# Kernel optimization log

Measured on AMD Instinct MI355X. Metric: run time of the kernel, lower is better.

Reference implementation:

```python
import jax, jax.numpy as jnp
import numpy as np

LOG_PROB_FACTOR = 0.5  # logProbFactor


def setup_inputs() -> dict:
    key = jax.random.key(0)
    ks = jax.random.split(key, 8)
    B, L, F, K = 2048, 512, 64, 2
    s = jax.random.randint(ks[0], (B, L), 0, K)
    W0 = jax.random.normal(ks[1], (K, F), jnp.float32) / np.sqrt(K).astype(np.float32)
    b0 = jnp.zeros((F,), jnp.float32)
    # fused LSTM weights, gate order (i, f, g, o); flax: dense_i no bias, dense_h has bias
    Wi = jax.random.normal(ks[2], (F, 4 * F), jnp.float32) / np.sqrt(F).astype(np.float32)
    Wh = jax.random.normal(ks[3], (F, 4 * F), jnp.float32) / np.sqrt(F).astype(np.float32)
    bh = jnp.zeros((4 * F,), jnp.float32)
    Wa = jax.random.normal(ks[4], (F, K), jnp.float32) / np.sqrt(F).astype(np.float32)
    ba = jnp.zeros((K,), jnp.float32)
    Wp = jax.random.normal(ks[5], (F, 1), jnp.float32) / np.sqrt(F).astype(np.float32)
    bp = jnp.zeros((1,), jnp.float32)
    return {"s": s, "W0": W0, "b0": b0, "Wi": Wi, "Wh": Wh, "bh": bh,
            "Wa": Wa, "ba": ba, "Wp": Wp, "bp": bp}


def _forward(s, W0, b0, Wi, Wh, bh, Wa, ba, Wp, bp):
    B, L = s.shape
    K, F = W0.shape
    # pad a leading zero token: input at step t is spin at site t-1
    s_pad = jnp.pad(s, ((0, 0), (1, 0)))                       # [B, L+1]
    x = jax.nn.one_hot(s_pad, K, dtype=W0.dtype) @ W0 + b0     # layer0: [B, L+1, F]
    xs = jnp.swapaxes(x, 0, 1)                                 # [L+1, B, F] time-major
    c0 = jnp.zeros((B, F), x.dtype)
    h0 = jnp.zeros((B, F), x.dtype)

    def step(carry, xt):
        c, h = carry
        g = xt @ Wi + h @ Wh + bh                              # [B, 4F]
        i, f, gg, o = jnp.split(g, 4, axis=-1)
        cn = jax.nn.sigmoid(f) * c + jax.nn.sigmoid(i) * jnp.tanh(gg)
        hn = jax.nn.sigmoid(o) * jnp.tanh(cn)
        return (cn, hn), hn

    _, ys = jax.lax.scan(step, (c0, h0), xs)                   # [L+1, B, F]

    logits = ys[:-1] @ Wa + ba                                 # [L, B, K]
    logp = jax.nn.log_softmax(logits, axis=-1) * LOG_PROB_FACTOR
    picked = jnp.take_along_axis(logp, s.T[..., None], axis=-1)[..., 0]  # [L, B]
    amp = picked.sum(axis=0)                                   # [B]
    phase = (ys[-1] @ Wp + bp)[..., 0]                         # [B]
    return amp + 1j * phase                                    # complex log-psi per sample


def reference(s, W0, b0, Wi, Wh, bh, Wa, ba, Wp, bp):
    return _forward(s, W0, b0, Wi, Wh, bh, Wa, ba, Wp, bp)
```

## Files before the change

kernel.cpp:

```cpp
#include <hip/hip_runtime.h>
#include <math.h>

typedef _Float16 f16x8 __attribute__((ext_vector_type(8)));
typedef float    f32x4 __attribute__((ext_vector_type(4)));
typedef _Float16 f16x2 __attribute__((ext_vector_type(2)));
typedef __fp16   fp16x2 __attribute__((ext_vector_type(2)));

#define B_TOT 2048
#define LSEQ  512
#define NS    16
#define LOG2E 1.44269504088896f
#define LN2   0.69314718055995f

#define MFMA16(A, B, C) __builtin_amdgcn_mfma_f32_16x16x32_f16((A), (B), (C), 0, 0, 0)

__device__ __forceinline__ unsigned int pkrtz(float a, float b) {
    fp16x2 p = __builtin_amdgcn_cvt_pkrtz(a, b);
    return __builtin_bit_cast(unsigned int, p);
}

__global__ __launch_bounds__(256, 1)
void lstm_v13_kernel(const int* __restrict__ s,
                     const float* __restrict__ W0, const float* __restrict__ b0,
                     const float* __restrict__ Wi, const float* __restrict__ Wh,
                     const float* __restrict__ bh, const float* __restrict__ Wa,
                     const float* __restrict__ ba, const float* __restrict__ Wp,
                     const float* __restrict__ bp, float* __restrict__ out)
{
    const int tid  = threadIdx.x;
    const int w    = tid >> 6;
    const int lane = tid & 63;
    const int n    = lane & 15;
    const int q    = lane >> 4;
    const int b0s  = blockIdx.x * NS;

    __shared__ __align__(16) unsigned int HhD[2][512];
    __shared__ unsigned short TOKB[LSEQ + 2];
    __shared__ unsigned char  SRAW[NS][LSEQ];
    __shared__ _Float16 DBUF[LSEQ][NS];
    __shared__ float PART[16][NS];

    for (int i = tid; i < NS * LSEQ; i += 256)
        SRAW[i >> 9][i & 511] = (unsigned char)s[(b0s + (i >> 9)) * LSEQ + (i & 511)];
    __syncthreads();
    for (int u = tid; u <= LSEQ; u += 256) {
        unsigned int mask = 0;
        if (u >= 1) {
            #pragma unroll
            for (int m = 0; m < NS; ++m)
                mask |= ((unsigned int)SRAW[m][u - 1]) << m;
        }
        TOKB[u] = (unsigned short)mask;
    }

    f16x8 awh[4][2];
    #pragma unroll
    for (int g = 0; g < 4; ++g) {
        const float sc  = (g == 2) ? (2.0f * LOG2E) : (-LOG2E);
        const int   col = 64 * g + 16 * w + n;
        #pragma unroll
        for (int c = 0; c < 2; ++c)
            #pragma unroll
            for (int j = 0; j < 8; ++j)
                awh[g][c][j] = (_Float16)(Wh[(32 * c + 8 * q + j) * 256 + col] * sc);
    }

    f16x8 awd[2];
    #pragma unroll
    for (int c = 0; c < 2; ++c)
        #pragma unroll
        for (int j = 0; j < 8; ++j) {
            int k = 32 * c + 8 * q + j;
            awd[c][j] = (_Float16)((n == 0) ? (Wa[2 * k + 1] - Wa[2 * k]) : 0.0f);
        }
    const float dba = ba[1] - ba[0];

    f32x4 p0q[4], dpq[4];
    {
        float a0[4][4], a1[4][4];
        #pragma unroll
        for (int g = 0; g < 4; ++g)
            #pragma unroll
            for (int r = 0; r < 4; ++r) {
                float bb = bh[64 * g + 16 * w + 4 * q + r];
                a0[g][r] = bb; a1[g][r] = bb;
            }
        for (int f = 0; f < 64; ++f) {
            float wb0 = W0[f]      + b0[f];
            float wb1 = W0[64 + f] + b0[f];
            #pragma unroll
            for (int g = 0; g < 4; ++g) {
                const float4 wi4 = *(const float4*)&Wi[f * 256 + 64 * g + 16 * w + 4 * q];
                #pragma unroll
                for (int r = 0; r < 4; ++r) {
                    float wi = (&wi4.x)[r];
                    a0[g][r] = fmaf(wb0, wi, a0[g][r]);
                    a1[g][r] = fmaf(wb1, wi, a1[g][r]);
                }
            }
        }
        #pragma unroll
        for (int g = 0; g < 4; ++g) {
            const float sc = (g == 2) ? (2.0f * LOG2E) : (-LOG2E);
            #pragma unroll
            for (int r = 0; r < 4; ++r) {
                p0q[g][r] = a0[g][r] * sc;
                dpq[g][r] = (a1[g][r] - a0[g][r]) * sc;
            }
        }
    }

    __syncthreads();

    const int wAddr = 4 * n + 64 * (q >> 1) + 128 * w + 2 * (q & 1);
    const int rAddr = 4 * n + 64 * (q & 1) + 128 * (q >> 1);

    float h4[4] = {0, 0, 0, 0}, c4[4] = {0, 0, 0, 0};
    f32x4 ci[4];
    #pragma unroll
    for (int g = 0; g < 4; ++g) ci[g] = p0q[g];

    float dpend = 0.0f;
    int   tpend = -1;

    #pragma unroll 4
    for (int v = 0; v <= LSEQ; ++v) {
        const int p = v & 1;
        unsigned int* __restrict__ hb = &HhD[p][0];

        uint2 hw;
        hw.x = pkrtz(h4[0], h4[1]);
        hw.y = pkrtz(h4[2], h4[3]);
        *(uint2*)&hb[wAddr] = hw;
        __syncthreads();

        if (tpend >= 0) {
            if (lane < 16) DBUF[tpend][n] = (_Float16)dpend;
            tpend = -1;
        }

        uint4 r0 = *(const uint4*)&hb[rAddr];
        uint4 r1 = *(const uint4*)&hb[rAddr + 256];
        const f16x8 bf0 = __builtin_bit_cast(f16x8, r0);
        const f16x8 bf1 = __builtin_bit_cast(f16x8, r1);

        const unsigned int tokm_next = (v < LSEQ) ? (unsigned int)TOKB[v + 1] : 0u;

        f32x4 acc0 = ci[0], acc1 = ci[1], acc2 = ci[2], acc3 = ci[3];
        acc0 = MFMA16(awh[0][0], bf0, acc0);
        acc1 = MFMA16(awh[1][0], bf0, acc1);
        acc2 = MFMA16(awh[2][0], bf0, acc2);
        acc3 = MFMA16(awh[3][0], bf0, acc3);
        acc0 = MFMA16(awh[0][1], bf1, acc0);
        acc1 = MFMA16(awh[1][1], bf1, acc1);
        acc2 = MFMA16(awh[2][1], bf1, acc2);
        acc3 = MFMA16(awh[3][1], bf1, acc3);

        if (v >= 1 && w == (v & 3)) {
            f32x4 da = (f32x4){dba, dba, dba, dba};
            da = MFMA16(awd[0], bf0, da);
            da = MFMA16(awd[1], bf1, da);
            dpend = da[0];
            tpend = v - 1;
        }

        const float sel = (float)((tokm_next >> n) & 1u);
        const f32x4 sel4 = {sel, sel, sel, sel};
        #pragma unroll
        for (int g = 0; g < 4; ++g)
            ci[g] = dpq[g] * sel4 + p0q[g];

        #pragma unroll
        for (int r = 0; r < 4; ++r) {
            float ei = __builtin_amdgcn_exp2f(acc0[r]);
            float ef = __builtin_amdgcn_exp2f(acc1[r]);
            float eg = __builtin_amdgcn_exp2f(acc2[r]);
            float eo = __builtin_amdgcn_exp2f(acc3[r]);
            float P  = (1.0f + ei) * (eg + 1.0f);
            float F  = 1.0f + ef;
            float R2 = __builtin_amdgcn_rcpf(P * F);
            float cn = fmaf(c4[r] * P, R2, (eg - 1.0f) * F * R2);
            c4[r] = cn;
            float ec = __builtin_amdgcn_exp2f(fminf(cn * (2.0f * LOG2E), 60.f));
            float Ro = __builtin_amdgcn_rcpf((1.0f + eo) * (ec + 1.0f));
            h4[r] = (ec - 1.0f) * Ro;
        }
    }

    if (tpend >= 0 && lane < 16) DBUF[tpend][n] = (_Float16)dpend;
    {
        uint2 hw;
        hw.x = pkrtz(h4[0], h4[1]);
        hw.y = pkrtz(h4[2], h4[3]);
        *(uint2*)&HhD[1][wAddr] = hw;
    }
    __syncthreads();

    {
        const int nn = tid & 15;
        const int ch = tid >> 4;
        float a = 0.0f;
        #pragma unroll 4
        for (int k = 0; k < 32; ++k) {
            int t = ch * 32 + k;
            float d = (float)DBUF[t][nn];
            float x = SRAW[nn][t] ? -d : d;
            float e = __builtin_amdgcn_exp2f(-fabsf(x) * LOG2E);
            a += fmaxf(x, 0.0f) + __builtin_amdgcn_logf(1.0f + e) * LN2;
        }
        PART[ch][nn] = a;
    }
    __syncthreads();

    if (tid < 16) {
        float ssum = 0.0f;
        #pragma unroll
        for (int c = 0; c < 16; ++c) ssum += PART[c][tid];
        out[b0s + tid] = -0.5f * ssum;
    }

    if (w == 0) {
        float ph = 0.0f;
        #pragma unroll
        for (int d = 0; d < 4; ++d) {
            unsigned int ua = HhD[1][4 * n + 128 * q + d];
            unsigned int ub = HhD[1][4 * n + 64 + 128 * q + d];
            f16x2 ha  = __builtin_bit_cast(f16x2, ua);
            f16x2 hb2 = __builtin_bit_cast(f16x2, ub);
            ph = fmaf((float)ha[0], Wp[16 * q + 2 * d],
                 fmaf((float)ha[1], Wp[16 * q + 2 * d + 1], ph));
            ph = fmaf((float)hb2[0], Wp[16 * q + 8 + 2 * d],
                 fmaf((float)hb2[1], Wp[16 * q + 8 + 2 * d + 1], ph));
        }
        ph += __shfl_xor(ph, 16, 64);
        ph += __shfl_xor(ph, 32, 64);
        if (q == 0) out[B_TOT + b0s + n] = ph + bp[0];
    }
}

extern "C" void kernel_launch(void* const* d_in, const int* in_sizes, int n_in,
                              void* d_out, int out_size, void* d_ws, size_t ws_size,
                              hipStream_t stream) {
    const int*   s  = (const int*)  d_in[0];
    const float* W0 = (const float*)d_in[1];
    const float* b0 = (const float*)d_in[2];
    const float* Wi = (const float*)d_in[3];
    const float* Wh = (const float*)d_in[4];
    const float* bh = (const float*)d_in[5];
    const float* Wa = (const float*)d_in[6];
    const float* ba = (const float*)d_in[7];
    const float* Wp = (const float*)d_in[8];
    const float* bp = (const float*)d_in[9];
    float* out = (float*)d_out;

    dim3 grid(B_TOT / NS);
    dim3 block(256);
    lstm_v13_kernel<<<grid, block, 0, stream>>>(s, W0, b0, Wi, Wh, bh,
                                                Wa, ba, Wp, bp, out);
}
```

Measured before the change: 320.7 us.

## Pack two independent 16-sample LSTM chains into each 512-thread block

Each block now runs two independent groups of 16 batch samples, one per 256-thread half, with separate shared-memory buffers indexed by chain. This halves the grid and doubles the block size, so each CU interleaves two recurrence chains and can hide the latency of MFMA, transcendental and LDS operations in the serial time loop. In exchange, the block-wide barrier now couples both chains every step, and fewer CUs are used overall.

```diff
diff --git a/kernel.cpp b/kernel.cpp
--- a/kernel.cpp
+++ b/kernel.cpp
@@ -9,6 +9,7 @@
 #define B_TOT 2048
 #define LSEQ  512
 #define NS    16
+#define NCH   2
 #define LOG2E 1.44269504088896f
 #define LN2   0.69314718055995f
 
@@ -19,8 +20,8 @@
     return __builtin_bit_cast(unsigned int, p);
 }
 
-__global__ __launch_bounds__(256, 1)
-void lstm_v13_kernel(const int* __restrict__ s,
+__global__ __launch_bounds__(512, 1)
+void lstm_v14_kernel(const int* __restrict__ s,
                      const float* __restrict__ W0, const float* __restrict__ b0,
                      const float* __restrict__ Wi, const float* __restrict__ Wh,
                      const float* __restrict__ bh, const float* __restrict__ Wa,
@@ -28,29 +29,31 @@
                      const float* __restrict__ bp, float* __restrict__ out)
 {
     const int tid  = threadIdx.x;
-    const int w    = tid >> 6;
+    const int ch   = tid >> 8;
+    const int ct   = tid & 255;
+    const int w    = ct >> 6;
     const int lane = tid & 63;
     const int n    = lane & 15;
     const int q    = lane >> 4;
-    const int b0s  = blockIdx.x * NS;
-
-    __shared__ __align__(16) unsigned int HhD[2][512];
-    __shared__ unsigned short TOKB[LSEQ + 2];
-    __shared__ unsigned char  SRAW[NS][LSEQ];
-    __shared__ _Float16 DBUF[LSEQ][NS];
-    __shared__ float PART[16][NS];
-
-    for (int i = tid; i < NS * LSEQ; i += 256)
-        SRAW[i >> 9][i & 511] = (unsigned char)s[(b0s + (i >> 9)) * LSEQ + (i & 511)];
-    __syncthreads();
-    for (int u = tid; u <= LSEQ; u += 256) {
+    const int b0s  = blockIdx.x * (NS * NCH) + ch * NS;
+
+    __shared__ __align__(16) unsigned int HhD[NCH][2][512];
+    __shared__ unsigned short TOKB[NCH][LSEQ + 2];
+    __shared__ unsigned char  SRAW[NCH][NS][LSEQ];
+    __shared__ _Float16 DBUF[NCH][LSEQ][NS];
+    __shared__ float PART[NCH][16][NS];
+
+    for (int i = ct; i < NS * LSEQ; i += 256)
+        SRAW[ch][i >> 9][i & 511] = (unsigned char)s[(b0s + (i >> 9)) * LSEQ + (i & 511)];
+    __syncthreads();
+    for (int u = ct; u <= LSEQ; u += 256) {
         unsigned int mask = 0;
         if (u >= 1) {
             #pragma unroll
             for (int m = 0; m < NS; ++m)
-                mask |= ((unsigned int)SRAW[m][u - 1]) << m;
-        }
-        TOKB[u] = (unsigned short)mask;
+                mask |= ((unsigned int)SRAW[ch][m][u - 1]) << m;
+        }
+        TOKB[ch][u] = (unsigned short)mask;
     }
 
     f16x8 awh[4][2];
@@ -126,7 +129,7 @@
     #pragma unroll 4
     for (int v = 0; v <= LSEQ; ++v) {
         const int p = v & 1;
-        unsigned int* __restrict__ hb = &HhD[p][0];
+        unsigned int* __restrict__ hb = &HhD[ch][p][0];
 
         uint2 hw;
         hw.x = pkrtz(h4[0], h4[1]);
@@ -135,7 +138,7 @@
         __syncthreads();
 
         if (tpend >= 0) {
-            if (lane < 16) DBUF[tpend][n] = (_Float16)dpend;
+            if (lane < 16) DBUF[ch][tpend][n] = (_Float16)dpend;
             tpend = -1;
         }
 
@@ -144,7 +147,7 @@
         const f16x8 bf0 = __builtin_bit_cast(f16x8, r0);
         const f16x8 bf1 = __builtin_bit_cast(f16x8, r1);
 
-        const unsigned int tokm_next = (v < LSEQ) ? (unsigned int)TOKB[v + 1] : 0u;
+        const unsigned int tokm_next = (v < LSEQ) ? (unsigned int)TOKB[ch][v + 1] : 0u;
 
         f32x4 acc0 = ci[0], acc1 = ci[1], acc2 = ci[2], acc3 = ci[3];
         acc0 = MFMA16(awh[0][0], bf0, acc0);
@@ -187,44 +190,44 @@
         }
     }
 
-    if (tpend >= 0 && lane < 16) DBUF[tpend][n] = (_Float16)dpend;
+    if (tpend >= 0 && lane < 16) DBUF[ch][tpend][n] = (_Float16)dpend;
     {
         uint2 hw;
         hw.x = pkrtz(h4[0], h4[1]);
         hw.y = pkrtz(h4[2], h4[3]);
-        *(uint2*)&HhD[1][wAddr] = hw;
+        *(uint2*)&HhD[ch][1][wAddr] = hw;
     }
     __syncthreads();
 
     {
-        const int nn = tid & 15;
-        const int ch = tid >> 4;
+        const int nn = ct & 15;
+        const int cc = ct >> 4;
         float a = 0.0f;
         #pragma unroll 4
         for (int k = 0; k < 32; ++k) {
-            int t = ch * 32 + k;
-            float d = (float)DBUF[t][nn];
-            float x = SRAW[nn][t] ? -d : d;
+            int t = cc * 32 + k;
+            float d = (float)DBUF[ch][t][nn];
+            float x = SRAW[ch][nn][t] ? -d : d;
             float e = __builtin_amdgcn_exp2f(-fabsf(x) * LOG2E);
             a += fmaxf(x, 0.0f) + __builtin_amdgcn_logf(1.0f + e) * LN2;
         }
-        PART[ch][nn] = a;
-    }
-    __syncthreads();
-
-    if (tid < 16) {
+        PART[ch][cc][nn] = a;
+    }
+    __syncthreads();
+
+    if (ct < 16) {
         float ssum = 0.0f;
         #pragma unroll
-        for (int c = 0; c < 16; ++c) ssum += PART[c][tid];
-        out[b0s + tid] = -0.5f * ssum;
+        for (int c = 0; c < 16; ++c) ssum += PART[ch][c][ct];
+        out[b0s + ct] = -0.5f * ssum;
     }
 
     if (w == 0) {
         float ph = 0.0f;
         #pragma unroll
         for (int d = 0; d < 4; ++d) {
-            unsigned int ua = HhD[1][4 * n + 128 * q + d];
-            unsigned int ub = HhD[1][4 * n + 64 + 128 * q + d];
+            unsigned int ua = HhD[ch][1][4 * n + 128 * q + d];
+            unsigned int ub = HhD[ch][1][4 * n + 64 + 128 * q + d];
             f16x2 ha  = __builtin_bit_cast(f16x2, ua);
             f16x2 hb2 = __builtin_bit_cast(f16x2, ub);
             ph = fmaf((float)ha[0], Wp[16 * q + 2 * d],
@@ -253,8 +256,8 @@
     const float* bp = (const float*)d_in[9];
     float* out = (float*)d_out;
 
-    dim3 grid(B_TOT / NS);
-    dim3 block(256);
-    lstm_v13_kernel<<<grid, block, 0, stream>>>(s, W0, b0, Wi, Wh, bh,
+    dim3 grid(B_TOT / (NS * NCH));
+    dim3 block(512);
+    lstm_v14_kernel<<<grid, block, 0, stream>>>(s, W0, b0, Wi, Wh, bh,
                                                 Wa, ba, Wp, bp, out);
 }
```

Result: slower. 425.5 us (+32.7%).

## Halve samples per block to double grid and split gate math across lanes

Applied to the files above, without the earlier changes.

Each block now handles 8 samples instead of 16, which doubles the grid to 256 blocks so every CU on the device gets work. The 16-column MFMA tile is reused with duplicated sample columns. Each lane now computes the nonlinear gate math for only 2 of its 4 accumulator rows, selected by the high bit of the column index, which halves the per-step elementwise work. The cost is that half of the MFMA throughput is spent on duplicate columns, and the reduction and DBUF indexing change with it.

```diff
diff --git a/kernel.cpp b/kernel.cpp
--- a/kernel.cpp
+++ b/kernel.cpp
@@ -8,7 +8,7 @@
 
 #define B_TOT 2048
 #define LSEQ  512
-#define NS    16
+#define NS    8
 #define LOG2E 1.44269504088896f
 #define LN2   0.69314718055995f
 
@@ -20,7 +20,7 @@
 }
 
 __global__ __launch_bounds__(256, 1)
-void lstm_v13_kernel(const int* __restrict__ s,
+void lstm_v16_kernel(const int* __restrict__ s,
                      const float* __restrict__ W0, const float* __restrict__ b0,
                      const float* __restrict__ Wi, const float* __restrict__ Wh,
                      const float* __restrict__ bh, const float* __restrict__ Wa,
@@ -32,13 +32,15 @@
     const int lane = tid & 63;
     const int n    = lane & 15;
     const int q    = lane >> 4;
+    const int ns   = n & 7;
+    const int hi   = n >> 3;
     const int b0s  = blockIdx.x * NS;
 
     __shared__ __align__(16) unsigned int HhD[2][512];
     __shared__ unsigned short TOKB[LSEQ + 2];
     __shared__ unsigned char  SRAW[NS][LSEQ];
     __shared__ _Float16 DBUF[LSEQ][NS];
-    __shared__ float PART[16][NS];
+    __shared__ float PART[32][NS];
 
     for (int i = tid; i < NS * LSEQ; i += 256)
         SRAW[i >> 9][i & 511] = (unsigned char)s[(b0s + (i >> 9)) * LSEQ + (i & 511)];
@@ -112,10 +114,10 @@
 
     __syncthreads();
 
-    const int wAddr = 4 * n + 64 * (q >> 1) + 128 * w + 2 * (q & 1);
-    const int rAddr = 4 * n + 64 * (q & 1) + 128 * (q >> 1);
-
-    float h4[4] = {0, 0, 0, 0}, c4[4] = {0, 0, 0, 0};
+    const int wAddr = 4 * ns + 64 * (q >> 1) + 128 * w + 2 * (q & 1) + hi;
+    const int rAddr = 4 * ns + 64 * (q & 1) + 128 * (q >> 1);
+
+    float h2[2] = {0, 0}, c2[2] = {0, 0};
     f32x4 ci[4];
     #pragma unroll
     for (int g = 0; g < 4; ++g) ci[g] = p0q[g];
@@ -128,14 +130,11 @@
         const int p = v & 1;
         unsigned int* __restrict__ hb = &HhD[p][0];
 
-        uint2 hw;
-        hw.x = pkrtz(h4[0], h4[1]);
-        hw.y = pkrtz(h4[2], h4[3]);
-        *(uint2*)&hb[wAddr] = hw;
+        hb[wAddr] = pkrtz(h2[0], h2[1]);
         __syncthreads();
 
         if (tpend >= 0) {
-            if (lane < 16) DBUF[tpend][n] = (_Float16)dpend;
+            if (lane < 8) DBUF[tpend][lane] = (_Float16)dpend;
             tpend = -1;
         }
 
@@ -164,58 +163,59 @@
             tpend = v - 1;
         }
 
-        const float sel = (float)((tokm_next >> n) & 1u);
+        const float sel = (float)((tokm_next >> ns) & 1u);
         const f32x4 sel4 = {sel, sel, sel, sel};
         #pragma unroll
         for (int g = 0; g < 4; ++g)
             ci[g] = dpq[g] * sel4 + p0q[g];
 
-        #pragma unroll
-        for (int r = 0; r < 4; ++r) {
-            float ei = __builtin_amdgcn_exp2f(acc0[r]);
-            float ef = __builtin_amdgcn_exp2f(acc1[r]);
-            float eg = __builtin_amdgcn_exp2f(acc2[r]);
-            float eo = __builtin_amdgcn_exp2f(acc3[r]);
+        const bool hb2 = (hi != 0);
+        float gi[2] = { hb2 ? acc0[2] : acc0[0], hb2 ? acc0[3] : acc0[1] };
+        float gf[2] = { hb2 ? acc1[2] : acc1[0], hb2 ? acc1[3] : acc1[1] };
+        float gg[2] = { hb2 ? acc2[2] : acc2[0], hb2 ? acc2[3] : acc2[1] };
+        float go[2] = { hb2 ? acc3[2] : acc3[0], hb2 ? acc3[3] : acc3[1] };
+
+        #pragma unroll
+        for (int rr = 0; rr < 2; ++rr) {
+            float ei = __builtin_amdgcn_exp2f(gi[rr]);
+            float ef = __builtin_amdgcn_exp2f(gf[rr]);
+            float eg = __builtin_amdgcn_exp2f(gg[rr]);
+            float eo = __builtin_amdgcn_exp2f(go[rr]);
             float P  = (1.0f + ei) * (eg + 1.0f);
             float F  = 1.0f + ef;
             float R2 = __builtin_amdgcn_rcpf(P * F);
-            float cn = fmaf(c4[r] * P, R2, (eg - 1.0f) * F * R2);
-            c4[r] = cn;
+            float cn = fmaf(c2[rr] * P, R2, (eg - 1.0f) * F * R2);
+            c2[rr] = cn;
             float ec = __builtin_amdgcn_exp2f(fminf(cn * (2.0f * LOG2E), 60.f));
             float Ro = __builtin_amdgcn_rcpf((1.0f + eo) * (ec + 1.0f));
-            h4[r] = (ec - 1.0f) * Ro;
-        }
-    }
-
-    if (tpend >= 0 && lane < 16) DBUF[tpend][n] = (_Float16)dpend;
+            h2[rr] = (ec - 1.0f) * Ro;
+        }
+    }
+
+    if (tpend >= 0 && lane < 8) DBUF[tpend][lane] = (_Float16)dpend;
+    HhD[1][wAddr] = pkrtz(h2[0], h2[1]);
+    __syncthreads();
+
     {
-        uint2 hw;
-        hw.x = pkrtz(h4[0], h4[1]);
-        hw.y = pkrtz(h4[2], h4[3]);
-        *(uint2*)&HhD[1][wAddr] = hw;
-    }
-    __syncthreads();
-
-    {
-        const int nn = tid & 15;
-        const int ch = tid >> 4;
+        const int nn = tid & 7;
+        const int cp = tid >> 3;
         float a = 0.0f;
         #pragma unroll 4
-        for (int k = 0; k < 32; ++k) {
-            int t = ch * 32 + k;
+        for (int k = 0; k < 16; ++k) {
+            int t = cp * 16 + k;
             float d = (float)DBUF[t][nn];
             float x = SRAW[nn][t] ? -d : d;
             float e = __builtin_amdgcn_exp2f(-fabsf(x) * LOG2E);
             a += fmaxf(x, 0.0f) + __builtin_amdgcn_logf(1.0f + e) * LN2;
         }
-        PART[ch][nn] = a;
-    }
-    __syncthreads();
-
-    if (tid < 16) {
+        PART[cp][nn] = a;
+    }
+    __syncthreads();
+
+    if (tid < 8) {
         float ssum = 0.0f;
         #pragma unroll
-        for (int c = 0; c < 16; ++c) ssum += PART[c][tid];
+        for (int c = 0; c < 32; ++c) ssum += PART[c][tid];
         out[b0s + tid] = -0.5f * ssum;
     }
 
@@ -223,18 +223,18 @@
         float ph = 0.0f;
         #pragma unroll
         for (int d = 0; d < 4; ++d) {
-            unsigned int ua = HhD[1][4 * n + 128 * q + d];
-            unsigned int ub = HhD[1][4 * n + 64 + 128 * q + d];
+            unsigned int ua = HhD[1][4 * ns + 128 * q + d];
+            unsigned int ub = HhD[1][4 * ns + 64 + 128 * q + d];
             f16x2 ha  = __builtin_bit_cast(f16x2, ua);
-            f16x2 hb2 = __builtin_bit_cast(f16x2, ub);
+            f16x2 hc  = __builtin_bit_cast(f16x2, ub);
             ph = fmaf((float)ha[0], Wp[16 * q + 2 * d],
                  fmaf((float)ha[1], Wp[16 * q + 2 * d + 1], ph));
-            ph = fmaf((float)hb2[0], Wp[16 * q + 8 + 2 * d],
-                 fmaf((float)hb2[1], Wp[16 * q + 8 + 2 * d + 1], ph));
+            ph = fmaf((float)hc[0], Wp[16 * q + 8 + 2 * d],
+                 fmaf((float)hc[1], Wp[16 * q + 8 + 2 * d + 1], ph));
         }
         ph += __shfl_xor(ph, 16, 64);
         ph += __shfl_xor(ph, 32, 64);
-        if (q == 0) out[B_TOT + b0s + n] = ph + bp[0];
+        if (q == 0 && n < 8) out[B_TOT + b0s + n] = ph + bp[0];
     }
 }
 
@@ -255,6 +255,6 @@
 
     dim3 grid(B_TOT / NS);
     dim3 block(256);
-    lstm_v13_kernel<<<grid, block, 0, stream>>>(s, W0, b0, Wi, Wh, bh,
+    lstm_v16_kernel<<<grid, block, 0, stream>>>(s, W0, b0, Wi, Wh, bh,
                                                 Wa, ba, Wp, bp, out);
 }
```

Result: faster. 277.1 us (-13.6%).

## Give each wavefront two independent sequences to drop per-step block barriers

Applied to the files above, without the earlier changes.

Before, four wavefronts split the gate columns for 16 sequences and had to sync at a block barrier on every timestep. Now each wavefront owns two sequences outright and holds all 16 gate tiles of Wh in registers. The hidden state is exchanged only through wave-private LDS, so the per-step __syncthreads disappears. The cost is 32 MFMAs per step for just two sequences, which wastes most of the MFMA N dimension, plus much higher register pressure. The grid grows to 256 blocks of 8 sequences.

```diff
diff --git a/kernel.cpp b/kernel.cpp
--- a/kernel.cpp
+++ b/kernel.cpp
@@ -3,12 +3,10 @@
 
 typedef _Float16 f16x8 __attribute__((ext_vector_type(8)));
 typedef float    f32x4 __attribute__((ext_vector_type(4)));
-typedef _Float16 f16x2 __attribute__((ext_vector_type(2)));
 typedef __fp16   fp16x2 __attribute__((ext_vector_type(2)));
 
 #define B_TOT 2048
 #define LSEQ  512
-#define NS    16
 #define LOG2E 1.44269504088896f
 #define LN2   0.69314718055995f
 
@@ -18,9 +16,15 @@
     fp16x2 p = __builtin_amdgcn_cvt_pkrtz(a, b);
     return __builtin_bit_cast(unsigned int, p);
 }
+__device__ __forceinline__ float f16lo(unsigned int u) {
+    return (float)__builtin_bit_cast(fp16x2, u)[0];
+}
+__device__ __forceinline__ float f16hi(unsigned int u) {
+    return (float)__builtin_bit_cast(fp16x2, u)[1];
+}
 
 __global__ __launch_bounds__(256, 1)
-void lstm_v13_kernel(const int* __restrict__ s,
+void lstm_v17_kernel(const int* __restrict__ s,
                      const float* __restrict__ W0, const float* __restrict__ b0,
                      const float* __restrict__ Wi, const float* __restrict__ Wh,
                      const float* __restrict__ bh, const float* __restrict__ Wa,
@@ -32,209 +36,186 @@
     const int lane = tid & 63;
     const int n    = lane & 15;
     const int q    = lane >> 4;
-    const int b0s  = blockIdx.x * NS;
-
-    __shared__ __align__(16) unsigned int HhD[2][512];
-    __shared__ unsigned short TOKB[LSEQ + 2];
-    __shared__ unsigned char  SRAW[NS][LSEQ];
-    __shared__ _Float16 DBUF[LSEQ][NS];
-    __shared__ float PART[16][NS];
-
-    for (int i = tid; i < NS * LSEQ; i += 256)
-        SRAW[i >> 9][i & 511] = (unsigned char)s[(b0s + (i >> 9)) * LSEQ + (i & 511)];
-    __syncthreads();
-    for (int u = tid; u <= LSEQ; u += 256) {
-        unsigned int mask = 0;
-        if (u >= 1) {
-            #pragma unroll
-            for (int m = 0; m < NS; ++m)
-                mask |= ((unsigned int)SRAW[m][u - 1]) << m;
-        }
-        TOKB[u] = (unsigned short)mask;
-    }
-
-    f16x8 awh[4][2];
+    const int ns   = n & 1;
+    const int kcpy = n >> 1;
+    const int c    = kcpy >> 1;
+    const int p    = kcpy & 1;
+    const int b0s  = blockIdx.x * 8 + w * 2;
+
+    __shared__ __align__(16) unsigned int HWX[4 * 64];
+    __shared__ unsigned char TOKW[4][LSEQ + 4];
+    __shared__ _Float16 DBUF[4][LSEQ][2];
+
     #pragma unroll
-    for (int g = 0; g < 4; ++g) {
-        const float sc  = (g == 2) ? (2.0f * LOG2E) : (-LOG2E);
-        const int   col = 64 * g + 16 * w + n;
-        #pragma unroll
-        for (int c = 0; c < 2; ++c)
-            #pragma unroll
-            for (int j = 0; j < 8; ++j)
-                awh[g][c][j] = (_Float16)(Wh[(32 * c + 8 * q + j) * 256 + col] * sc);
-    }
-
-    f16x8 awd[2];
-    #pragma unroll
-    for (int c = 0; c < 2; ++c)
-        #pragma unroll
-        for (int j = 0; j < 8; ++j) {
-            int k = 32 * c + 8 * q + j;
-            awd[c][j] = (_Float16)((n == 0) ? (Wa[2 * k + 1] - Wa[2 * k]) : 0.0f);
-        }
-    const float dba = ba[1] - ba[0];
-
-    f32x4 p0q[4], dpq[4];
+    for (int j = 0; j < 8; ++j) {
+        int t = lane + 64 * j;
+        int s0 = s[(b0s + 0) * LSEQ + t];
+        int s1 = s[(b0s + 1) * LSEQ + t];
+        TOKW[w][t] = (unsigned char)(s0 | (s1 << 1));
+    }
+    if (lane == 0) TOKW[w][LSEQ] = 0;
+
+    f32x4 p0q[16], dpq[16];
     {
-        float a0[4][4], a1[4][4];
-        #pragma unroll
-        for (int g = 0; g < 4; ++g)
+        f32x4 A0[16], A1[16];
+        #pragma unroll
+        for (int t = 0; t < 16; ++t)
             #pragma unroll
             for (int r = 0; r < 4; ++r) {
-                float bb = bh[64 * g + 16 * w + 4 * q + r];
-                a0[g][r] = bb; a1[g][r] = bb;
+                float bb = bh[16 * t + 4 * q + r];
+                A0[t][r] = bb; A1[t][r] = bb;
             }
+        #pragma unroll 2
         for (int f = 0; f < 64; ++f) {
             float wb0 = W0[f]      + b0[f];
             float wb1 = W0[64 + f] + b0[f];
             #pragma unroll
-            for (int g = 0; g < 4; ++g) {
-                const float4 wi4 = *(const float4*)&Wi[f * 256 + 64 * g + 16 * w + 4 * q];
+            for (int t = 0; t < 16; ++t) {
+                const float4 wi4 = *(const float4*)&Wi[f * 256 + 16 * t + 4 * q];
                 #pragma unroll
                 for (int r = 0; r < 4; ++r) {
-                    float wi = (&wi4.x)[r];
-                    a0[g][r] = fmaf(wb0, wi, a0[g][r]);
-                    a1[g][r] = fmaf(wb1, wi, a1[g][r]);
+                    float wv = (&wi4.x)[r];
+                    A0[t][r] = fmaf(wb0, wv, A0[t][r]);
+                    A1[t][r] = fmaf(wb1, wv, A1[t][r]);
                 }
             }
         }
         #pragma unroll
-        for (int g = 0; g < 4; ++g) {
-            const float sc = (g == 2) ? (2.0f * LOG2E) : (-LOG2E);
+        for (int t = 0; t < 16; ++t) {
+            const float sc = ((t >> 2) == 2) ? (2.0f * LOG2E) : (-LOG2E);
             #pragma unroll
             for (int r = 0; r < 4; ++r) {
-                p0q[g][r] = a0[g][r] * sc;
-                dpq[g][r] = (a1[g][r] - a0[g][r]) * sc;
+                p0q[t][r] = A0[t][r] * sc;
+                dpq[t][r] = (A1[t][r] - A0[t][r]) * sc;
             }
         }
     }
 
-    __syncthreads();
-
-    const int wAddr = 4 * n + 64 * (q >> 1) + 128 * w + 2 * (q & 1);
-    const int rAddr = 4 * n + 64 * (q & 1) + 128 * (q >> 1);
-
-    float h4[4] = {0, 0, 0, 0}, c4[4] = {0, 0, 0, 0};
-    f32x4 ci[4];
+    f16x8 awh[16][2];
     #pragma unroll
-    for (int g = 0; g < 4; ++g) ci[g] = p0q[g];
-
-    float dpend = 0.0f;
-    int   tpend = -1;
-
-    #pragma unroll 4
+    for (int t = 0; t < 16; ++t) {
+        const float sc = ((t >> 2) == 2) ? (2.0f * LOG2E) : (-LOG2E);
+        const int col = 16 * t + n;
+        #pragma unroll
+        for (int h = 0; h < 2; ++h)
+            #pragma unroll
+            for (int j = 0; j < 8; ++j)
+                awh[t][h][j] = (_Float16)(Wh[(32 * h + 8 * q + j) * 256 + col] * sc);
+    }
+    f16x8 awd[2];
+    #pragma unroll
+    for (int h = 0; h < 2; ++h)
+        #pragma unroll
+        for (int j = 0; j < 8; ++j) {
+            int kx = 32 * h + 8 * q + j;
+            awd[h][j] = (_Float16)((n == 0) ? (Wa[2 * kx + 1] - Wa[2 * kx]) : 0.0f);
+        }
+    const float dba = ba[1] - ba[0];
+
+    const int wA  = w * 64 + 32 * ns + 8 * c + 2 * q + p;
+    const int rA0 = w * 64 + 32 * ns + 4 * q;
+
+    float h2[2] = {0.f, 0.f}, c2[2] = {0.f, 0.f};
+    float selc = 0.f;
+
     for (int v = 0; v <= LSEQ; ++v) {
-        const int p = v & 1;
-        unsigned int* __restrict__ hb = &HhD[p][0];
-
-        uint2 hw;
-        hw.x = pkrtz(h4[0], h4[1]);
-        hw.y = pkrtz(h4[2], h4[3]);
-        *(uint2*)&hb[wAddr] = hw;
-        __syncthreads();
-
-        if (tpend >= 0) {
-            if (lane < 16) DBUF[tpend][n] = (_Float16)dpend;
-            tpend = -1;
-        }
-
-        uint4 r0 = *(const uint4*)&hb[rAddr];
-        uint4 r1 = *(const uint4*)&hb[rAddr + 256];
+        HWX[wA] = pkrtz(h2[0], h2[1]);
+        const unsigned int tk = TOKW[w][v];
+        const uint4 r0 = *(const uint4*)&HWX[rA0];
+        const uint4 r1 = *(const uint4*)&HWX[rA0 + 16];
         const f16x8 bf0 = __builtin_bit_cast(f16x8, r0);
         const f16x8 bf1 = __builtin_bit_cast(f16x8, r1);
 
-        const unsigned int tokm_next = (v < LSEQ) ? (unsigned int)TOKB[v + 1] : 0u;
-
-        f32x4 acc0 = ci[0], acc1 = ci[1], acc2 = ci[2], acc3 = ci[3];
-        acc0 = MFMA16(awh[0][0], bf0, acc0);
-        acc1 = MFMA16(awh[1][0], bf0, acc1);
-        acc2 = MFMA16(awh[2][0], bf0, acc2);
-        acc3 = MFMA16(awh[3][0], bf0, acc3);
-        acc0 = MFMA16(awh[0][1], bf1, acc0);
-        acc1 = MFMA16(awh[1][1], bf1, acc1);
-        acc2 = MFMA16(awh[2][1], bf1, acc2);
-        acc3 = MFMA16(awh[3][1], bf1, acc3);
-
-        if (v >= 1 && w == (v & 3)) {
-            f32x4 da = (f32x4){dba, dba, dba, dba};
-            da = MFMA16(awd[0], bf0, da);
-            da = MFMA16(awd[1], bf1, da);
-            dpend = da[0];
-            tpend = v - 1;
-        }
-
-        const float sel = (float)((tokm_next >> n) & 1u);
-        const f32x4 sel4 = {sel, sel, sel, sel};
-        #pragma unroll
-        for (int g = 0; g < 4; ++g)
-            ci[g] = dpq[g] * sel4 + p0q[g];
-
-        #pragma unroll
-        for (int r = 0; r < 4; ++r) {
-            float ei = __builtin_amdgcn_exp2f(acc0[r]);
-            float ef = __builtin_amdgcn_exp2f(acc1[r]);
-            float eg = __builtin_amdgcn_exp2f(acc2[r]);
-            float eo = __builtin_amdgcn_exp2f(acc3[r]);
+        const f32x4 sel4 = {selc, selc, selc, selc};
+        f32x4 acc[16];
+        #pragma unroll
+        for (int t = 0; t < 16; ++t)
+            acc[t] = MFMA16(awh[t][0], bf0, dpq[t] * sel4 + p0q[t]);
+        #pragma unroll
+        for (int t = 0; t < 16; ++t)
+            acc[t] = MFMA16(awh[t][1], bf1, acc[t]);
+
+        f32x4 da = {dba, dba, dba, dba};
+        da = MFMA16(awd[0], bf0, da);
+        da = MFMA16(awd[1], bf1, da);
+
+        selc = (float)((tk >> ns) & 1u);
+
+        float gl[4], gh[4];
+        #pragma unroll
+        for (int g = 0; g < 4; ++g) {
+            float pl0 = p ? acc[4*g+0][2] : acc[4*g+0][0];
+            float pl1 = p ? acc[4*g+1][2] : acc[4*g+1][0];
+            float pl2 = p ? acc[4*g+2][2] : acc[4*g+2][0];
+            float pl3 = p ? acc[4*g+3][2] : acc[4*g+3][0];
+            float ph0 = p ? acc[4*g+0][3] : acc[4*g+0][1];
+            float ph1 = p ? acc[4*g+1][3] : acc[4*g+1][1];
+            float ph2 = p ? acc[4*g+2][3] : acc[4*g+2][1];
+            float ph3 = p ? acc[4*g+3][3] : acc[4*g+3][1];
+            float la = (c & 1) ? pl1 : pl0;
+            float lb = (c & 1) ? pl3 : pl2;
+            gl[g] = (c & 2) ? lb : la;
+            float ha = (c & 1) ? ph1 : ph0;
+            float hb = (c & 1) ? ph3 : ph2;
+            gh[g] = (c & 2) ? hb : ha;
+        }
+
+        #pragma unroll
+        for (int jj = 0; jj < 2; ++jj) {
+            float gi = jj ? gh[0] : gl[0];
+            float gf = jj ? gh[1] : gl[1];
+            float gg = jj ? gh[2] : gl[2];
+            float go = jj ? gh[3] : gl[3];
+            float ei = __builtin_amdgcn_exp2f(gi);
+            float ef = __builtin_amdgcn_exp2f(gf);
+            float eg = __builtin_amdgcn_exp2f(gg);
+            float eo = __builtin_amdgcn_exp2f(go);
             float P  = (1.0f + ei) * (eg + 1.0f);
             float F  = 1.0f + ef;
             float R2 = __builtin_amdgcn_rcpf(P * F);
-            float cn = fmaf(c4[r] * P, R2, (eg - 1.0f) * F * R2);
-            c4[r] = cn;
+            float cn = fmaf(c2[jj] * P, R2, (eg - 1.0f) * F * R2);
+            c2[jj] = cn;
             float ec = __builtin_amdgcn_exp2f(fminf(cn * (2.0f * LOG2E), 60.f));
             float Ro = __builtin_amdgcn_rcpf((1.0f + eo) * (ec + 1.0f));
-            h4[r] = (ec - 1.0f) * Ro;
-        }
-    }
-
-    if (tpend >= 0 && lane < 16) DBUF[tpend][n] = (_Float16)dpend;
+            h2[jj] = (ec - 1.0f) * Ro;
+        }
+
+        if (v >= 1 && lane < 2) DBUF[w][v - 1][lane] = (_Float16)da[0];
+    }
+
     {
-        uint2 hw;
-        hw.x = pkrtz(h4[0], h4[1]);
-        hw.y = pkrtz(h4[2], h4[3]);
-        *(uint2*)&HhD[1][wAddr] = hw;
-    }
-    __syncthreads();
+        float aa0 = 0.f, aa1 = 0.f;
+        #pragma unroll 2
+        for (int j = 0; j < 8; ++j) {
+            int t = lane + 64 * j;
+            unsigned int dd = *(const unsigned int*)&DBUF[w][t][0];
+            float d0 = f16lo(dd), d1 = f16hi(dd);
+            unsigned int tk = TOKW[w][t];
+            float x0 = (tk & 1u) ? -d0 : d0;
+            float x1 = (tk & 2u) ? -d1 : d1;
+            float e0 = __builtin_amdgcn_exp2f(-fabsf(x0) * LOG2E);
+            float e1 = __builtin_amdgcn_exp2f(-fabsf(x1) * LOG2E);
+            aa0 += fmaxf(x0, 0.f) + __builtin_amdgcn_logf(1.0f + e0) * LN2;
+            aa1 += fmaxf(x1, 0.f) + __builtin_amdgcn_logf(1.0f + e1) * LN2;
+        }
+        #pragma unroll
+        for (int m = 1; m < 64; m <<= 1) {
+            aa0 += __shfl_xor(aa0, m, 64);
+            aa1 += __shfl_xor(aa1, m, 64);
+        }
+        if (lane == 0) {
+            out[b0s + 0] = -0.5f * aa0;
+            out[b0s + 1] = -0.5f * aa1;
+        }
+    }
 
     {
-        const int nn = tid & 15;
-        const int ch = tid >> 4;
-        float a = 0.0f;
-        #pragma unroll 4
-        for (int k = 0; k < 32; ++k) {
-            int t = ch * 32 + k;
-            float d = (float)DBUF[t][nn];
-            float x = SRAW[nn][t] ? -d : d;
-            float e = __builtin_amdgcn_exp2f(-fabsf(x) * LOG2E);
-            a += fmaxf(x, 0.0f) + __builtin_amdgcn_logf(1.0f + e) * LN2;
-        }
-        PART[ch][nn] = a;
-    }
-    __syncthreads();
-
-    if (tid < 16) {
-        float ssum = 0.0f;
-        #pragma unroll
-        for (int c = 0; c < 16; ++c) ssum += PART[c][tid];
-        out[b0s + tid] = -0.5f * ssum;
-    }
-
-    if (w == 0) {
-        float ph = 0.0f;
-        #pragma unroll
-        for (int d = 0; d < 4; ++d) {
-            unsigned int ua = HhD[1][4 * n + 128 * q + d];
-            unsigned int ub = HhD[1][4 * n + 64 + 128 * q + d];
-            f16x2 ha  = __builtin_bit_cast(f16x2, ua);
-            f16x2 hb2 = __builtin_bit_cast(f16x2, ub);
-            ph = fmaf((float)ha[0], Wp[16 * q + 2 * d],
-                 fmaf((float)ha[1], Wp[16 * q + 2 * d + 1], ph));
-            ph = fmaf((float)hb2[0], Wp[16 * q + 8 + 2 * d],
-                 fmaf((float)hb2[1], Wp[16 * q + 8 + 2 * d + 1], ph));
-        }
-        ph += __shfl_xor(ph, 16, 64);
-        ph += __shfl_xor(ph, 32, 64);
-        if (q == 0) out[B_TOT + b0s + n] = ph + bp[0];
+        const int f = 16 * c + 4 * q + 2 * p;
+        float ph = fmaf(h2[0], Wp[f], h2[1] * Wp[f + 1]);
+        #pragma unroll
+        for (int m = 2; m < 64; m <<= 1)
+            ph += __shfl_xor(ph, m, 64);
+        if (lane < 2) out[B_TOT + b0s + lane] = ph + bp[0];
     }
 }
 
@@ -253,8 +234,8 @@
     const float* bp = (const float*)d_in[9];
     float* out = (float*)d_out;
 
-    dim3 grid(B_TOT / NS);
+    dim3 grid(B_TOT / 8);
     dim3 block(256);
-    lstm_v13_kernel<<<grid, block, 0, stream>>>(s, W0, b0, Wi, Wh, bh,
+    lstm_v17_kernel<<<grid, block, 0, stream>>>(s, W0, b0, Wi, Wh, bh,
                                                 Wa, ba, Wp, bp, out);
 }
```

Result: slower. 815.1 us (+154.2%).
